# Kernel tuning notes

Hardware: AMD Instinct MI355X
Metric: run time of the kernel (lower is better)

Reference implementation:

```python
import jax, jax.numpy as jnp
import numpy as np

EMBED_DIM = 4096
NUM_Q_HEADS = 32
NUM_KV_HEADS = 8
HEAD_DIM = EMBED_DIM // NUM_Q_HEADS  # 128
GROUP = NUM_Q_HEADS // NUM_KV_HEADS  # 4
KV_SEQ_LEN = 1024
BATCH = 2
SEQ = 1024
THETA = 10000.0


def _rope(x, positions):
    # x: (B, T, H, D) with interleaved real/imag pairs along D (torch view_as_complex layout)
    half = x.shape[-1] // 2
    inv_freq = 1.0 / (THETA ** (jnp.arange(half, dtype=jnp.float32) / half))
    ang = positions[:, None].astype(jnp.float32) * inv_freq[None, :]  # (T, half)
    cos = jnp.cos(ang)[None, :, None, :].astype(x.dtype)
    sin = jnp.sin(ang)[None, :, None, :].astype(x.dtype)
    xr = x.reshape(*x.shape[:-1], half, 2)
    x0, x1 = xr[..., 0], xr[..., 1]
    o0 = x0 * cos - x1 * sin
    o1 = x0 * sin + x1 * cos
    return jnp.stack([o0, o1], axis=-1).reshape(x.shape)


def setup_inputs() -> dict:
    key = jax.random.key(0)
    ks = jax.random.split(key, 5)
    s_in = 1.0 / np.sqrt(EMBED_DIM)
    return {
        "x": jax.random.normal(ks[0], (BATCH, SEQ, EMBED_DIM), dtype=jnp.float32),
        "Wq": jax.random.normal(ks[1], (EMBED_DIM, EMBED_DIM), dtype=jnp.float32) * s_in,
        "Wk": jax.random.normal(ks[2], (NUM_KV_HEADS * HEAD_DIM, EMBED_DIM), dtype=jnp.float32) * s_in,
        "Wv": jax.random.normal(ks[3], (NUM_KV_HEADS * HEAD_DIM, EMBED_DIM), dtype=jnp.float32) * s_in,
        "Wo": jax.random.normal(ks[4], (EMBED_DIM, EMBED_DIM), dtype=jnp.float32) * s_in,
        "cache_k": jnp.zeros((BATCH, 2 * KV_SEQ_LEN, NUM_KV_HEADS, HEAD_DIM), dtype=jnp.float32),
        "cache_v": jnp.zeros((BATCH, 2 * KV_SEQ_LEN, NUM_KV_HEADS, HEAD_DIM), dtype=jnp.float32),
        "start_pos": 0,
    }


def reference(x, Wq, Wk, Wv, Wo, cache_k, cache_v, start_pos):
    B, T, C = x.shape
    end_pos = start_pos + T
    scale = 1.0 / np.sqrt(HEAD_DIM)

    q = (x @ Wq.T).reshape(B, T, NUM_Q_HEADS, HEAD_DIM)
    k = (x @ Wk.T).reshape(B, T, NUM_KV_HEADS, HEAD_DIM)
    v = (x @ Wv.T).reshape(B, T, NUM_KV_HEADS, HEAD_DIM)

    pos = start_pos + jnp.arange(T)
    q = _rope(q, pos)
    k = _rope(k, pos)

    # KV cache append (writes are detached in the original)
    cache_k = cache_k.at[:, start_pos:end_pos].set(jax.lax.stop_gradient(k))
    cache_v = cache_v.at[:, start_pos:end_pos].set(jax.lax.stop_gradient(v))
    k_full = cache_k[:, :end_pos]  # (B, S, Hkv, D)
    v_full = cache_v[:, :end_pos]

    # GQA without materializing repeated KV heads:
    # q head h attends kv head h // GROUP (matches repeat_interleave layout)
    q5 = q.transpose(0, 2, 1, 3).reshape(B, NUM_KV_HEADS, GROUP, T, HEAD_DIM)
    kh = k_full.transpose(0, 2, 1, 3)  # (B, Hkv, S, D)
    vh = v_full.transpose(0, 2, 1, 3)

    scores = jnp.einsum('bhgtd,bhsd->bhgts', q5, kh) * scale  # (B,Hkv,G,T,S)
    visible = jnp.arange(end_pos)[None, :] <= (start_pos + jnp.arange(T))[:, None]  # (T,S)
    scores = jnp.where(visible[None, None, None], scores, jnp.finfo(scores.dtype).min)
    probs = jax.nn.softmax(scores, axis=-1)
    ctx = jnp.einsum('bhgts,bhsd->bhgtd', probs, vh)

    out = ctx.reshape(B, NUM_Q_HEADS, T, HEAD_DIM).transpose(0, 2, 1, 3).reshape(B, T, C)
    return out @ Wo.T
```

## Files before the change

### kernel.cpp

```cpp
#include <hip/hip_runtime.h>
#include <stdint.h>

typedef unsigned short u16;
typedef __attribute__((ext_vector_type(8))) short short8x;
typedef __attribute__((ext_vector_type(4))) float floatx4;

#define TOKENS 2048
#define EMBED  4096
#define QKVN   6144
#define T_SEQ  1024
#define SMAX   2048
#define NQH    32
#define NKVH   8
#define HD     128

static __device__ __forceinline__ u16 f2b(float f) {
    union { float f; uint32_t u; } v; v.f = f;
    uint32_t r = v.u + 0x7fffu + ((v.u >> 16) & 1u);
    return (u16)(r >> 16);
}
static __device__ __forceinline__ float b2f(u16 h) {
    union { uint32_t u; float f; } v; v.u = ((uint32_t)h) << 16; return v.f;
}

static __device__ __forceinline__ void gload_lds16(const u16* g, u16* l) {
    __builtin_amdgcn_global_load_lds(
        (const __attribute__((address_space(1))) uint32_t*)g,
        (__attribute__((address_space(3))) uint32_t*)l, 16, 0, 0);
}

#define CSEG0 2097152
#define CSEG1 6291456
#define CSEG2 7340032
#define CSEG3 8388608
#define CSEG4 12582912
__global__ void convert_all_kernel(const float* __restrict__ x,  const float* __restrict__ Wq,
                                   const float* __restrict__ Wk, const float* __restrict__ Wv,
                                   const float* __restrict__ Wo,
                                   u16* __restrict__ xb, u16* __restrict__ wqkv,
                                   u16* __restrict__ wob) {
    int i = blockIdx.x * blockDim.x + threadIdx.x;
    if (i >= CSEG4) return;
    const float4* src; uint2* dst; int off;
    if (i < CSEG0)      { src = (const float4*)x;  dst = (uint2*)xb;   off = i; }
    else if (i < CSEG1) { src = (const float4*)Wq; dst = (uint2*)wqkv; off = i - CSEG0; }
    else if (i < CSEG2) { src = (const float4*)Wk; dst = (uint2*)wqkv + 4194304; off = i - CSEG1; }
    else if (i < CSEG3) { src = (const float4*)Wv; dst = (uint2*)wqkv + 5242880; off = i - CSEG2; }
    else                { src = (const float4*)Wo; dst = (uint2*)wob;  off = i - CSEG3; }
    float4 f = src[off];
    union { u16 h[4]; uint2 v; } o;
    o.h[0] = f2b(f.x); o.h[1] = f2b(f.y); o.h[2] = f2b(f.z); o.h[3] = f2b(f.w);
    dst[off] = o.v;
}

#define HB(BUF, MAT, H) (lds + (((BUF) * 4 + (MAT) * 2 + (H)) * 8192))
#define STAGE(BUF, MAT, H, KT) do { \
    const u16* _g0 = (MAT) ? gB[H][0] : gA[H][0]; \
    const u16* _g1 = (MAT) ? gB[H][1] : gA[H][1]; \
    gload_lds16(_g0 + (size_t)(KT) * 64, HB(BUF, MAT, H) + dOff0); \
    gload_lds16(_g1 + (size_t)(KT) * 64, HB(BUF, MAT, H) + dOff1); \
} while (0)
#define WAIT4 asm volatile("s_waitcnt vmcnt(4)" ::: "memory")
#define WAIT0 asm volatile("s_waitcnt vmcnt(0)" ::: "memory")
#define NOSTG ((void)0)
#define LDAF(CBUF, AH, KK) do { const u16* _p = HB(CBUF, 0, AH); \
    _Pragma("unroll") \
    for (int _mi = 0; _mi < 4; _mi++) \
        af[_mi] = *(const short8x*)(_p + offA[_mi][KK]); } while (0)
#define LDBF(CBUF, KK) do { \
    const u16* _p0 = HB(CBUF, 1, 0); \
    const u16* _p1 = HB(CBUF, 1, 1); \
    bf[0] = *(const short8x*)(_p0 + offB[0][KK]); \
    bf[1] = *(const short8x*)(_p0 + offB[1][KK]); \
    bf[2] = *(const short8x*)(_p1 + offB[0][KK]); \
    bf[3] = *(const short8x*)(_p1 + offB[1][KK]); } while (0)
#define NOLDB ((void)0)
#define PHASE(CBUF, AH, KK, LOADB, STAGES, ENDW) do { \
    LDAF(CBUF, AH, KK); \
    LOADB; \
    STAGES; \
    __builtin_amdgcn_s_barrier(); \
    asm volatile("s_waitcnt lgkmcnt(0)" ::: "memory"); \
    __builtin_amdgcn_sched_barrier(0); \
    __builtin_amdgcn_s_setprio(1); \
    _Pragma("unroll") \
    for (int _mi = 0; _mi < 4; _mi++) \
        _Pragma("unroll") \
        for (int _nj = 0; _nj < 4; _nj++) \
            acc[AH][_mi][_nj] = __builtin_amdgcn_mfma_f32_16x16x32_bf16( \
                af[_mi], bf[_nj], acc[AH][_mi][_nj], 0, 0, 0); \
    __builtin_amdgcn_s_setprio(0); \
    ENDW; \
    __builtin_amdgcn_s_barrier(); \
    __builtin_amdgcn_sched_barrier(0); \
} while (0)

__global__ __launch_bounds__(512, 1) void gemm256_kernel(
    const u16* __restrict__ A, const u16* __restrict__ Bw,
    u16* __restrict__ Cv, int N, int K) {
    extern __shared__ __align__(16) u16 lds[];
    const int tid = threadIdx.x;
    const int lane = tid & 63, w = tid >> 6;
    const int quad = lane >> 4, lc = lane & 15;
    const int wm = w >> 2, wn = w & 3;
    const int Mbase = blockIdx.y * 256, Nbase = blockIdx.x * 256;

    const int r8 = lane >> 3;
    const int sl = (lane & 7) ^ r8;
    const int srow = w * 8 + r8;
    const u16* gA[2][2];
    const u16* gB[2][2];
#pragma unroll
    for (int H = 0; H < 2; H++)
#pragma unroll
        for (int L = 0; L < 2; L++) {
            gA[H][L] = A  + (size_t)(Mbase + H * 128 + L * 64 + srow) * K + sl * 8;
            gB[H][L] = Bw + (size_t)(Nbase + H * 128 + L * 64 + srow) * K + sl * 8;
        }
    const int dOff0 = w * 8 * 64;
    const int dOff1 = (64 + w * 8) * 64;

    int offA[4][2], offB[2][2];
    const int xsw = lc & 7;
#pragma unroll
    for (int mi = 0; mi < 4; mi++)
#pragma unroll
        for (int kk = 0; kk < 2; kk++)
            offA[mi][kk] = (wm * 64 + mi * 16 + lc) * 64 + (((kk * 4 + quad) ^ xsw) * 8);
#pragma unroll
    for (int ni = 0; ni < 2; ni++)
#pragma unroll
        for (int kk = 0; kk < 2; kk++)
            offB[ni][kk] = (wn * 32 + ni * 16 + lc) * 64 + (((kk * 4 + quad) ^ xsw) * 8);

    floatx4 acc[2][4][4] = {};
    short8x af[4];
    short8x bf[4];

    STAGE(0, 0, 0, 0);
    STAGE(0, 1, 0, 0);
    STAGE(0, 0, 1, 0);
    STAGE(0, 1, 1, 0);
    STAGE(1, 0, 0, 1);
    STAGE(1, 1, 0, 1);
    WAIT4;
    __builtin_amdgcn_s_barrier();
    __builtin_amdgcn_sched_barrier(0);

    const int NT = K >> 6;
    for (int t = 0; t < NT - 2; t += 2) {
        PHASE(0, 0, 0, LDBF(0, 0), STAGE(1, 0, 1, t + 1); STAGE(1, 1, 1, t + 1), NOSTG);
        PHASE(0, 1, 0, NOLDB, NOSTG, NOSTG);
        PHASE(0, 0, 1, LDBF(0, 1), NOSTG, NOSTG);
        PHASE(0, 1, 1, NOLDB, STAGE(0, 0, 0, t + 2); STAGE(0, 1, 0, t + 2), WAIT4);
        PHASE(1, 0, 0, LDBF(1, 0), STAGE(0, 0, 1, t + 2); STAGE(0, 1, 1, t + 2), NOSTG);
        PHASE(1, 1, 0, NOLDB, NOSTG, NOSTG);
        PHASE(1, 0, 1, LDBF(1, 1), NOSTG, NOSTG);
        PHASE(1, 1, 1, NOLDB, STAGE(1, 0, 0, t + 3); STAGE(1, 1, 0, t + 3), WAIT4);
    }
    PHASE(0, 0, 0, LDBF(0, 0), STAGE(1, 0, 1, NT - 1); STAGE(1, 1, 1, NT - 1), NOSTG);
    PHASE(0, 1, 0, NOLDB, NOSTG, NOSTG);
    PHASE(0, 0, 1, LDBF(0, 1), NOSTG, NOSTG);
    PHASE(0, 1, 1, NOLDB, NOSTG, WAIT0);
    PHASE(1, 0, 0, LDBF(1, 0), NOSTG, NOSTG);
    PHASE(1, 1, 0, NOLDB, NOSTG, NOSTG);
    PHASE(1, 0, 1, LDBF(1, 1), NOSTG, NOSTG);
    PHASE(1, 1, 1, NOLDB, NOSTG, NOSTG);

#pragma unroll
    for (int AH = 0; AH < 2; AH++)
#pragma unroll
        for (int mi = 0; mi < 4; mi++) {
            const int row0 = Mbase + AH * 128 + wm * 64 + mi * 16 + quad * 4;
#pragma unroll
            for (int nj = 0; nj < 4; nj++) {
                const int col = Nbase + (nj >> 1) * 128 + wn * 32 + (nj & 1) * 16 + lc;
#pragma unroll
                for (int r = 0; r < 4; r++)
                    Cv[(size_t)(row0 + r) * N + col] = f2b(acc[AH][mi][nj][r]);
            }
        }
}
#undef HB
#undef STAGE
#undef LDAF
#undef LDBF
#undef NOLDB
#undef PHASE

#define HA2(BUF, H) (lds + (BUF) * 24576 + (H) * 4096)
#define HBB2(BUF)   (lds + (BUF) * 24576 + 8192)
#define STGA2(BUF, H, KT) gload_lds16(gA2[H] + (size_t)(KT) * 64, HA2(BUF, H) + dOffW)
#define STGB2(BUF, KT) do { \
    _Pragma("unroll") \
    for (int _L = 0; _L < 4; _L++) \
        gload_lds16(gB2[_L] + (size_t)(KT) * 64, HBB2(BUF) + _L * 4096 + dOffW); \
} while (0)
#define WAIT5 asm volatile("s_waitcnt vmcnt(5)" ::: "memory")
#define LDA2(CBUF, AH) do { const u16* _p = HA2(CBUF, AH); \
    _Pragma("unroll") \
    for (int _mi = 0; _mi < 2; _mi++) { \
        af2[_mi][0] = *(const short8x*)(_p + offA2[_mi][0]); \
        af2[_mi][1] = *(const short8x*)(_p + offA2[_mi][1]); } } while (0)
#define LDB2(CBUF) do { const u16* _p = HBB2(CBUF); \
    _Pragma("unroll") \
    for (int _nj = 0; _nj < 4; _nj++) { \
        bf2[_nj][0] = *(const short8x*)(_p + offB2[_nj][0]); \
        bf2[_nj][1] = *(const short8x*)(_p + offB2[_nj][1]); } } while (0)
#define PHASE2(CBUF, AH, LOADS, STAGES, ENDW) do { \
    LOADS; \
    STAGES; \
    __builtin_amdgcn_s_barrier(); \
    asm volatile("s_waitcnt lgkmcnt(0)" ::: "memory"); \
    __builtin_amdgcn_sched_barrier(0); \
    __builtin_amdgcn_s_setprio(1); \
    _Pragma("unroll") \
    for (int _kk = 0; _kk < 2; _kk++) \
        _Pragma("unroll") \
        for (int _mi = 0; _mi < 2; _mi++) \
            _Pragma("unroll") \
            for (int _nj = 0; _nj < 4; _nj++) \
                acc2[AH][_mi][_nj] = __builtin_amdgcn_mfma_f32_16x16x32_bf16( \
                    af2[_mi][_kk], bf2[_nj][_kk], acc2[AH][_mi][_nj], 0, 0, 0); \
    __builtin_amdgcn_s_setprio(0); \
    ENDW; \
    __builtin_amdgcn_s_barrier(); \
    __builtin_amdgcn_sched_barrier(0); \
} while (0)

__global__ __launch_bounds__(512, 1) void gemmko_kernel(
    const u16* __restrict__ A, const u16* __restrict__ Bw,
    float* __restrict__ C, int N, int K) {
    extern __shared__ __align__(16) u16 lds[];
    const int tid = threadIdx.x;
    const int lane = tid & 63, w = tid >> 6;
    const int quad = lane >> 4, lc = lane & 15;
    const int wm = (w >> 2) & 1, wn = w & 3;
    const int Mbase = blockIdx.y * 128, Nbase = blockIdx.x * 256;

    const int r8 = lane >> 3;
    const int sl = (lane & 7) ^ r8;
    const int srow = w * 8 + r8;
    const u16* gA2[2];
    const u16* gB2[4];
#pragma unroll
    for (int H = 0; H < 2; H++)
        gA2[H] = A + (size_t)(Mbase + H * 64 + srow) * K + sl * 8;
#pragma unroll
    for (int L = 0; L < 4; L++)
        gB2[L] = Bw + (size_t)(Nbase + L * 64 + srow) * K + sl * 8;
    const int dOffW = w * 512;

    int offA2[2][2], offB2[4][2];
    const int xsw = lc & 7;
#pragma unroll
    for (int mi = 0; mi < 2; mi++)
#pragma unroll
        for (int kk = 0; kk < 2; kk++)
            offA2[mi][kk] = (wm * 32 + mi * 16 + lc) * 64 + (((kk * 4 + quad) ^ xsw) * 8);
#pragma unroll
    for (int nj = 0; nj < 4; nj++)
#pragma unroll
        for (int kk = 0; kk < 2; kk++)
            offB2[nj][kk] = (wn * 64 + nj * 16 + lc) * 64 + (((kk * 4 + quad) ^ xsw) * 8);

    floatx4 acc2[2][2][4] = {};
    short8x af2[2][2], bf2[4][2];

    STGA2(0, 0, 0); STGA2(0, 1, 0); STGB2(0, 0);
    STGA2(1, 0, 1); STGB2(1, 1);
    WAIT5;
    __builtin_amdgcn_s_barrier();
    __builtin_amdgcn_sched_barrier(0);

    const int NT = K >> 6;
    for (int t = 0; t < NT - 2; t += 2) {
        PHASE2(0, 0, LDA2(0, 0); LDB2(0), STGA2(1, 1, t + 1), NOSTG);
        PHASE2(0, 1, LDA2(0, 1), STGA2(0, 0, t + 2); STGB2(0, t + 2), WAIT5);
        PHASE2(1, 0, LDA2(1, 0); LDB2(1), STGA2(0, 1, t + 2), NOSTG);
        PHASE2(1, 1, LDA2(1, 1), STGA2(1, 0, t + 3); STGB2(1, t + 3), WAIT5);
    }
    PHASE2(0, 0, LDA2(0, 0); LDB2(0), STGA2(1, 1, NT - 1), NOSTG);
    PHASE2(0, 1, LDA2(0, 1), NOSTG, WAIT0);
    PHASE2(1, 0, LDA2(1, 0); LDB2(1), NOSTG, NOSTG);
    PHASE2(1, 1, LDA2(1, 1), NOSTG, NOSTG);

#pragma unroll
    for (int AH = 0; AH < 2; AH++)
#pragma unroll
        for (int mi = 0; mi < 2; mi++) {
            const int row0 = Mbase + AH * 64 + wm * 32 + mi * 16 + quad * 4;
#pragma unroll
            for (int nj = 0; nj < 4; nj++) {
                const int col = Nbase + wn * 64 + nj * 16 + lc;
#pragma unroll
                for (int r = 0; r < 4; r++)
                    C[(size_t)(row0 + r) * N + col] = acc2[AH][mi][nj][r];
            }
        }
}
#undef HA2
#undef HBB2
#undef STGA2
#undef STGB2
#undef WAIT5
#undef LDA2
#undef LDB2
#undef PHASE2
#undef WAIT4
#undef WAIT0
#undef NOSTG

__global__ void cache_prefix_kernel(const float* __restrict__ ck, const float* __restrict__ cv,
                                    const int* __restrict__ sp,
                                    u16* __restrict__ kh, u16* __restrict__ vt8) {
    int spos = sp[0];
    long total = (long)2 * spos * NKVH * HD;
    for (long i = (long)blockIdx.x * blockDim.x + threadIdx.x; i < total; i += (long)gridDim.x * blockDim.x) {
        long d = i % HD, rest = i / HD;
        long g = rest % NKVH; rest /= NKVH;
        long s = rest % spos; long b = rest / spos;
        float kv = ck[((b * SMAX + s) * NKVH + g) * HD + d];
        kh[((b * NKVH + g) * SMAX + s) * HD + d] = f2b(kv);
        float vv = cv[((b * SMAX + s) * NKVH + g) * HD + d];
        vt8[(size_t)(b * NKVH + g) * SMAX * HD + (s >> 3) * 1024 + d * 8 + (s & 7)] = f2b(vv);
    }
}

__global__ void rope_qk_kernel(const u16* __restrict__ qkvb, const int* __restrict__ sp,
                               u16* __restrict__ qh, u16* __restrict__ kh) {
    int spos = sp[0];
    int idx = blockIdx.x * blockDim.x + threadIdx.x;
    int tok = idx / 2560;
    int u = idx - tok * 2560;
    int b = tok >> 10, t = tok & 1023;
    float pos = (float)(spos + t);
    const u16* src = qkvb + (size_t)tok * QKVN;
    const float kScale = 0.08838834764831845f;
    const float kLog = -0.20762050593045857f;
    if (u < 2048) {
        int h = u >> 6, i = u & 63;
        float ang = pos * exp2f((float)i * kLog);
        float cs = cosf(ang), sn = sinf(ang);
        float x0 = b2f(src[h * HD + 2 * i]), x1 = b2f(src[h * HD + 2 * i + 1]);
        size_t dst = (((size_t)(b * NQH + h) * T_SEQ) + t) * HD + 2 * i;
        qh[dst]     = f2b((x0 * cs - x1 * sn) * kScale);
        qh[dst + 1] = f2b((x0 * sn + x1 * cs) * kScale);
    } else {
        int u2 = u - 2048;
        int g = u2 >> 6, i = u2 & 63;
        float ang = pos * exp2f((float)i * kLog);
        float cs = cosf(ang), sn = sinf(ang);
        float x0 = b2f(src[EMBED + g * HD + 2 * i]), x1 = b2f(src[EMBED + g * HD + 2 * i + 1]);
        size_t dst = (((size_t)(b * NKVH + g) * SMAX) + spos + t) * HD + 2 * i;
        kh[dst]     = f2b(x0 * cs - x1 * sn);
        kh[dst + 1] = f2b(x0 * sn + x1 * cs);
    }
}

__global__ __launch_bounds__(256) void vpack_kernel(const u16* __restrict__ qkvb,
                                                    const int* __restrict__ sp,
                                                    u16* __restrict__ vt8) {
    __shared__ u16 lds[16 * 136];
    int spos = sp[0];
    int tile = blockIdx.x;
    int t16 = tile & 63;
    int g = (tile >> 6) & 7;
    int b = tile >> 9;
    int tok0 = t16 * 16;
    int tid = threadIdx.x;
    {
        int srow = tid >> 4, dc8 = (tid & 15) * 8;
        const u16* src = qkvb + (size_t)(b * T_SEQ + tok0 + srow) * QKVN + 5120 + g * HD + dc8;
        *(uint4*)(lds + srow * 136 + dc8) = *(const uint4*)src;
    }
    __syncthreads();
    int d = tid & 127, half = tid >> 7;
    u16* vpg = vt8 + (size_t)(b * NKVH + g) * SMAX * HD;
    int s0 = spos + tok0;
    u16 val[8];
#pragma unroll
    for (int k = 0; k < 8; k++) val[k] = lds[(half * 8 + k) * 136 + d];
    if ((s0 & 7) == 0) {
        union { u16 h[8]; uint4 u; } pk;
#pragma unroll
        for (int k = 0; k < 8; k++) pk.h[k] = val[k];
        *(uint4*)(vpg + (size_t)((s0 >> 3) + half) * 1024 + d * 8) = pk.u;
    } else {
#pragma unroll
        for (int k = 0; k < 8; k++) {
            int s = s0 + half * 8 + k;
            vpg[(size_t)(s >> 3) * 1024 + d * 8 + (s & 7)] = val[k];
        }
    }
}

__global__ __launch_bounds__(256, 2) void attn_kernel(
    const u16* __restrict__ qh, const u16* __restrict__ kh,
    const u16* __restrict__ vt8, const int* __restrict__ sp,
    u16* __restrict__ ctx) {
    extern __shared__ __align__(16) char smem[];
    int spos = sp[0];
    int tid = threadIdx.x, w = tid >> 6, lane = tid & 63;
    int quad = lane >> 4, lc = lane & 15;
    int tile = blockIdx.x;
    int j = 63 - (tile & 63);
    int g = (tile >> 6) & 7;
    int b = tile >> 9;
    int qbase = j * 16;

    const u16* kp = kh + (size_t)(b * NKVH + g) * SMAX * HD;
    const u16* vp = vt8 + (size_t)(b * NKVH + g) * SMAX * HD;

    short8x qf[4][4];
#pragma unroll
    for (int m = 0; m < 4; m++) {
        const u16* qp = qh + ((size_t)(b * NQH + g * 4 + m) * T_SEQ + qbase + lc) * HD + quad * 8;
#pragma unroll
        for (int dc = 0; dc < 4; dc++)
            qf[m][dc] = *(const short8x*)(qp + dc * 32);
    }
    short8x ones;
#pragma unroll
    for (int jj = 0; jj < 8; jj++) ones[jj] = (short)0x3F80;

    floatx4 o[4][8] = {};
    floatx4 lacc[4] = {};
    int rowpos = spos + qbase + quad * 4;
    int nch = (spos + qbase + 16 + 63) >> 6;
    u16* pw = (u16*)smem + w * 4608;

    for (int c = w; c < nch; c += 4) {
        int koff = c * 64;
#pragma unroll
        for (int st = 0; st < 4; st++) {
            const u16* kr = kp + (size_t)(koff + st * 16 + lc) * HD + quad * 8;
            floatx4 sc[4] = {};
#pragma unroll
            for (int dc = 0; dc < 4; dc++) {
                short8x kf = *(const short8x*)(kr + dc * 32);
#pragma unroll
                for (int m = 0; m < 4; m++)
                    sc[m] = __builtin_amdgcn_mfma_f32_16x16x32_bf16(qf[m][dc], kf, sc[m], 0, 0, 0);
            }
            int skey = koff + st * 16 + lc;
#pragma unroll
            for (int m = 0; m < 4; m++)
#pragma unroll
                for (int r = 0; r < 4; r++) {
                    float p = (skey <= rowpos + r) ? __expf(sc[m][r]) : 0.0f;
                    pw[m * 1152 + (quad * 4 + r) * 72 + st * 16 + lc] = f2b(p);
                }
        }
        asm volatile("s_waitcnt lgkmcnt(0)" ::: "memory");
#pragma unroll
        for (int hf = 0; hf < 2; hf++) {
            short8x pf[4];
#pragma unroll
            for (int m = 0; m < 4; m++)
                pf[m] = *(const short8x*)(pw + m * 1152 + lc * 72 + hf * 32 + quad * 8);
#pragma unroll
            for (int m = 0; m < 4; m++)
                lacc[m] = __builtin_amdgcn_mfma_f32_16x16x32_bf16(pf[m], ones, lacc[m], 0, 0, 0);
            const u16* vbase = vp + ((size_t)koff << 7) + (size_t)(hf * 4 + quad) * 1024 + lc * 8;
#pragma unroll
            for (int dc8 = 0; dc8 < 8; dc8++) {
                short8x vf = *(const short8x*)(vbase + dc8 * 128);
#pragma unroll
                for (int m = 0; m < 4; m++)
                    o[m][dc8] = __builtin_amdgcn_mfma_f32_16x16x32_bf16(pf[m], vf, o[m][dc8], 0, 0, 0);
            }
        }
    }

    float* obuf = (float*)smem;
    float* lbuf = (float*)(smem + 33792);
    for (int ph = 0; ph < 4; ph++) {
        __syncthreads();
        if (w == ph) {
            if (ph == 0) {
#pragma unroll
                for (int m = 0; m < 4; m++) {
#pragma unroll
                    for (int dc8 = 0; dc8 < 8; dc8++)
#pragma unroll
                        for (int r = 0; r < 4; r++)
                            obuf[(m * 16 + quad * 4 + r) * 132 + dc8 * 16 + lc] = o[m][dc8][r];
#pragma unroll
                    for (int r = 0; r < 4; r++) lbuf[m * 16 + quad * 4 + r] = lacc[m][r];
                }
            } else {
#pragma unroll
                for (int m = 0; m < 4; m++) {
#pragma unroll
                    for (int dc8 = 0; dc8 < 8; dc8++)
#pragma unroll
                        for (int r = 0; r < 4; r++)
                            obuf[(m * 16 + quad * 4 + r) * 132 + dc8 * 16 + lc] += o[m][dc8][r];
#pragma unroll
                    for (int r = 0; r < 4; r++) lbuf[m * 16 + quad * 4 + r] += lacc[m][r];
                }
            }
        }
    }
    __syncthreads();

    int row = tid >> 2;
    int m = row >> 4;
    int cb = (tid & 3) * 32;
    float inv = 1.0f / lbuf[row];
    int token = qbase + (row & 15);
    size_t base = ((size_t)(b * T_SEQ + token) * NQH + g * 4 + m) * HD + cb;
#pragma unroll
    for (int v4 = 0; v4 < 4; v4++) {
        union { u16 h[8]; uint4 u; } pk;
#pragma unroll
        for (int jj = 0; jj < 8; jj++)
            pk.h[jj] = f2b(obuf[row * 132 + cb + v4 * 8 + jj] * inv);
        *(uint4*)(ctx + base + v4 * 8) = pk.u;
    }
}

extern "C" void kernel_launch(void* const* d_in, const int* in_sizes, int n_in,
                              void* d_out, int out_size, void* d_ws, size_t ws_size,
                              hipStream_t stream) {
    const float* x  = (const float*)d_in[0];
    const float* Wq = (const float*)d_in[1];
    const float* Wk = (const float*)d_in[2];
    const float* Wv = (const float*)d_in[3];
    const float* Wo = (const float*)d_in[4];
    const float* ck = (const float*)d_in[5];
    const float* cv = (const float*)d_in[6];
    const int*   sp = (const int*)d_in[7];

    char* p = (char*)d_ws;
    u16* xb   = (u16*)p;
    u16* qh   = xb;
    p += (size_t)TOKENS * EMBED * 2;
    u16* wqkv = (u16*)p; p += (size_t)QKVN * EMBED * 2;
    u16* wob  = (u16*)p; p += (size_t)EMBED * EMBED * 2;
    u16* qkvb = (u16*)p;
    u16* ctx  = qkvb;
    p += (size_t)TOKENS * QKVN * 2;
    u16* kh   = (u16*)p; p += (size_t)2 * NKVH * SMAX * HD * 2;
    u16* vt8  = (u16*)p;

    static int gemm_attr = 0;
    if (!gemm_attr) {
        (void)hipFuncSetAttribute(reinterpret_cast<const void*>(&gemm256_kernel),
                                  hipFuncAttributeMaxDynamicSharedMemorySize, 131072);
        (void)hipFuncSetAttribute(reinterpret_cast<const void*>(&gemmko_kernel),
                                  hipFuncAttributeMaxDynamicSharedMemorySize, 98304);
        gemm_attr = 1;
    }

    convert_all_kernel<<<(CSEG4 + 255) / 256, 256, 0, stream>>>(x, Wq, Wk, Wv, Wo, xb, wqkv, wob);
    gemm256_kernel<<<dim3(QKVN / 256, TOKENS / 256), 512, 131072, stream>>>(xb, wqkv, qkvb, QKVN, EMBED);
    cache_prefix_kernel<<<256, 256, 0, stream>>>(ck, cv, sp, kh, vt8);
    rope_qk_kernel<<<TOKENS * 2560 / 256, 256, 0, stream>>>(qkvb, sp, qh, kh);
    vpack_kernel<<<1024, 256, 0, stream>>>(qkvb, sp, vt8);
    attn_kernel<<<1024, 256, 36864, stream>>>(qh, kh, vt8, sp, ctx);
    gemmko_kernel<<<dim3(EMBED / 256, TOKENS / 128), 512, 98304, stream>>>(ctx, wob, (float*)d_out, EMBED, EMBED);
}
```

Baseline: 337.2 us.

## Reshape QKV GEMM tile to 256x192 so the grid fills all CUs

Each block of the QKV projection GEMM now covers 192 output columns instead of 256. That gives a grid of 256 blocks instead of 192, so every CU on the device gets one block and the partial last wave goes away. The B-tile staging, LDS layout, fragment offsets, accumulators and epilogue are rewritten for three 64-row B slices, and the LDS allocation shrinks. Both GEMM kernels also replace the explicit lgkmcnt(0) wait and sched_barrier around barriers with compiler memory fences. That hands LDS wait placement to the compiler, trading a smaller per-block tile (less reuse) for better CU coverage.

```diff
diff --git a/kernel.cpp b/kernel.cpp
--- a/kernel.cpp
+++ b/kernel.cpp
@@ -53,46 +53,46 @@
     dst[off] = o.v;
 }
 
-#define HB(BUF, MAT, H) (lds + (((BUF) * 4 + (MAT) * 2 + (H)) * 8192))
-#define STAGE(BUF, MAT, H, KT) do { \
-    const u16* _g0 = (MAT) ? gB[H][0] : gA[H][0]; \
-    const u16* _g1 = (MAT) ? gB[H][1] : gA[H][1]; \
-    gload_lds16(_g0 + (size_t)(KT) * 64, HB(BUF, MAT, H) + dOff0); \
-    gload_lds16(_g1 + (size_t)(KT) * 64, HB(BUF, MAT, H) + dOff1); \
-} while (0)
-#define WAIT4 asm volatile("s_waitcnt vmcnt(4)" ::: "memory")
+#define FENCE asm volatile("" ::: "memory")
+#define WAIT5 asm volatile("s_waitcnt vmcnt(5)" ::: "memory")
 #define WAIT0 asm volatile("s_waitcnt vmcnt(0)" ::: "memory")
 #define NOSTG ((void)0)
-#define LDAF(CBUF, AH, KK) do { const u16* _p = HB(CBUF, 0, AH); \
+#define NOLDB ((void)0)
+
+#define HBA(BUF, H) (lds + (BUF) * 28672 + (H) * 8192)
+#define HBB(BUF)    (lds + (BUF) * 28672 + 16384)
+#define STGA(BUF, H, KT) do { \
+    gload_lds16(gA[H][0] + (size_t)(KT) * 64, HBA(BUF, H) + dOffW); \
+    gload_lds16(gA[H][1] + (size_t)(KT) * 64, HBA(BUF, H) + 4096 + dOffW); \
+} while (0)
+#define STGB(BUF, KT) do { \
+    _Pragma("unroll") \
+    for (int _L = 0; _L < 3; _L++) \
+        gload_lds16(gBv[_L] + (size_t)(KT) * 64, HBB(BUF) + _L * 4096 + dOffW); \
+} while (0)
+#define LDAF(CBUF, AH, KK) do { const u16* _p = HBA(CBUF, AH); \
     _Pragma("unroll") \
     for (int _mi = 0; _mi < 4; _mi++) \
         af[_mi] = *(const short8x*)(_p + offA[_mi][KK]); } while (0)
-#define LDBF(CBUF, KK) do { \
-    const u16* _p0 = HB(CBUF, 1, 0); \
-    const u16* _p1 = HB(CBUF, 1, 1); \
-    bf[0] = *(const short8x*)(_p0 + offB[0][KK]); \
-    bf[1] = *(const short8x*)(_p0 + offB[1][KK]); \
-    bf[2] = *(const short8x*)(_p1 + offB[0][KK]); \
-    bf[3] = *(const short8x*)(_p1 + offB[1][KK]); } while (0)
-#define NOLDB ((void)0)
+#define LDBF(CBUF, KK) do { const u16* _p = HBB(CBUF); \
+    _Pragma("unroll") \
+    for (int _nj = 0; _nj < 3; _nj++) \
+        bf[_nj] = *(const short8x*)(_p + offB[_nj][KK]); } while (0)
 #define PHASE(CBUF, AH, KK, LOADB, STAGES, ENDW) do { \
     LDAF(CBUF, AH, KK); \
     LOADB; \
     STAGES; \
-    __builtin_amdgcn_s_barrier(); \
-    asm volatile("s_waitcnt lgkmcnt(0)" ::: "memory"); \
-    __builtin_amdgcn_sched_barrier(0); \
+    FENCE; __builtin_amdgcn_s_barrier(); FENCE; \
     __builtin_amdgcn_s_setprio(1); \
     _Pragma("unroll") \
     for (int _mi = 0; _mi < 4; _mi++) \
         _Pragma("unroll") \
-        for (int _nj = 0; _nj < 4; _nj++) \
+        for (int _nj = 0; _nj < 3; _nj++) \
             acc[AH][_mi][_nj] = __builtin_amdgcn_mfma_f32_16x16x32_bf16( \
                 af[_mi], bf[_nj], acc[AH][_mi][_nj], 0, 0, 0); \
     __builtin_amdgcn_s_setprio(0); \
     ENDW; \
-    __builtin_amdgcn_s_barrier(); \
-    __builtin_amdgcn_sched_barrier(0); \
+    FENCE; __builtin_amdgcn_s_barrier(); FENCE; \
 } while (0)
 
 __global__ __launch_bounds__(512, 1) void gemm256_kernel(
@@ -103,24 +103,24 @@
     const int lane = tid & 63, w = tid >> 6;
     const int quad = lane >> 4, lc = lane & 15;
     const int wm = w >> 2, wn = w & 3;
-    const int Mbase = blockIdx.y * 256, Nbase = blockIdx.x * 256;
+    const int Mbase = blockIdx.y * 256, Nbase = blockIdx.x * 192;
 
     const int r8 = lane >> 3;
     const int sl = (lane & 7) ^ r8;
     const int srow = w * 8 + r8;
     const u16* gA[2][2];
-    const u16* gB[2][2];
+    const u16* gBv[3];
 #pragma unroll
     for (int H = 0; H < 2; H++)
 #pragma unroll
-        for (int L = 0; L < 2; L++) {
-            gA[H][L] = A  + (size_t)(Mbase + H * 128 + L * 64 + srow) * K + sl * 8;
-            gB[H][L] = Bw + (size_t)(Nbase + H * 128 + L * 64 + srow) * K + sl * 8;
-        }
-    const int dOff0 = w * 8 * 64;
-    const int dOff1 = (64 + w * 8) * 64;
-
-    int offA[4][2], offB[2][2];
+        for (int L = 0; L < 2; L++)
+            gA[H][L] = A + (size_t)(Mbase + H * 128 + L * 64 + srow) * K + sl * 8;
+#pragma unroll
+    for (int L = 0; L < 3; L++)
+        gBv[L] = Bw + (size_t)(Nbase + L * 64 + srow) * K + sl * 8;
+    const int dOffW = w * 512;
+
+    int offA[4][2], offB[3][2];
     const int xsw = lc & 7;
 #pragma unroll
     for (int mi = 0; mi < 4; mi++)
@@ -128,37 +128,32 @@
         for (int kk = 0; kk < 2; kk++)
             offA[mi][kk] = (wm * 64 + mi * 16 + lc) * 64 + (((kk * 4 + quad) ^ xsw) * 8);
 #pragma unroll
-    for (int ni = 0; ni < 2; ni++)
+    for (int nj = 0; nj < 3; nj++)
 #pragma unroll
         for (int kk = 0; kk < 2; kk++)
-            offB[ni][kk] = (wn * 32 + ni * 16 + lc) * 64 + (((kk * 4 + quad) ^ xsw) * 8);
-
-    floatx4 acc[2][4][4] = {};
+            offB[nj][kk] = (wn * 48 + nj * 16 + lc) * 64 + (((kk * 4 + quad) ^ xsw) * 8);
+
+    floatx4 acc[2][4][3] = {};
     short8x af[4];
-    short8x bf[4];
-
-    STAGE(0, 0, 0, 0);
-    STAGE(0, 1, 0, 0);
-    STAGE(0, 0, 1, 0);
-    STAGE(0, 1, 1, 0);
-    STAGE(1, 0, 0, 1);
-    STAGE(1, 1, 0, 1);
-    WAIT4;
-    __builtin_amdgcn_s_barrier();
-    __builtin_amdgcn_sched_barrier(0);
+    short8x bf[3];
+
+    STGA(0, 0, 0); STGA(0, 1, 0); STGB(0, 0);
+    STGA(1, 0, 1); STGB(1, 1);
+    WAIT5;
+    FENCE; __builtin_amdgcn_s_barrier(); FENCE;
 
     const int NT = K >> 6;
     for (int t = 0; t < NT - 2; t += 2) {
-        PHASE(0, 0, 0, LDBF(0, 0), STAGE(1, 0, 1, t + 1); STAGE(1, 1, 1, t + 1), NOSTG);
+        PHASE(0, 0, 0, LDBF(0, 0), STGA(1, 1, t + 1), NOSTG);
         PHASE(0, 1, 0, NOLDB, NOSTG, NOSTG);
         PHASE(0, 0, 1, LDBF(0, 1), NOSTG, NOSTG);
-        PHASE(0, 1, 1, NOLDB, STAGE(0, 0, 0, t + 2); STAGE(0, 1, 0, t + 2), WAIT4);
-        PHASE(1, 0, 0, LDBF(1, 0), STAGE(0, 0, 1, t + 2); STAGE(0, 1, 1, t + 2), NOSTG);
+        PHASE(0, 1, 1, NOLDB, STGA(0, 0, t + 2); STGB(0, t + 2), WAIT5);
+        PHASE(1, 0, 0, LDBF(1, 0), STGA(0, 1, t + 2), NOSTG);
         PHASE(1, 1, 0, NOLDB, NOSTG, NOSTG);
         PHASE(1, 0, 1, LDBF(1, 1), NOSTG, NOSTG);
-        PHASE(1, 1, 1, NOLDB, STAGE(1, 0, 0, t + 3); STAGE(1, 1, 0, t + 3), WAIT4);
-    }
-    PHASE(0, 0, 0, LDBF(0, 0), STAGE(1, 0, 1, NT - 1); STAGE(1, 1, 1, NT - 1), NOSTG);
+        PHASE(1, 1, 1, NOLDB, STGA(1, 0, t + 3); STGB(1, t + 3), WAIT5);
+    }
+    PHASE(0, 0, 0, LDBF(0, 0), STGA(1, 1, NT - 1), NOSTG);
     PHASE(0, 1, 0, NOLDB, NOSTG, NOSTG);
     PHASE(0, 0, 1, LDBF(0, 1), NOSTG, NOSTG);
     PHASE(0, 1, 1, NOLDB, NOSTG, WAIT0);
@@ -173,19 +168,20 @@
         for (int mi = 0; mi < 4; mi++) {
             const int row0 = Mbase + AH * 128 + wm * 64 + mi * 16 + quad * 4;
 #pragma unroll
-            for (int nj = 0; nj < 4; nj++) {
-                const int col = Nbase + (nj >> 1) * 128 + wn * 32 + (nj & 1) * 16 + lc;
+            for (int nj = 0; nj < 3; nj++) {
+                const int col = Nbase + wn * 48 + nj * 16 + lc;
 #pragma unroll
                 for (int r = 0; r < 4; r++)
                     Cv[(size_t)(row0 + r) * N + col] = f2b(acc[AH][mi][nj][r]);
             }
         }
 }
-#undef HB
-#undef STAGE
+#undef HBA
+#undef HBB
+#undef STGA
+#undef STGB
 #undef LDAF
 #undef LDBF
-#undef NOLDB
 #undef PHASE
 
 #define HA2(BUF, H) (lds + (BUF) * 24576 + (H) * 4096)
@@ -196,7 +192,7 @@
     for (int _L = 0; _L < 4; _L++) \
         gload_lds16(gB2[_L] + (size_t)(KT) * 64, HBB2(BUF) + _L * 4096 + dOffW); \
 } while (0)
-#define WAIT5 asm volatile("s_waitcnt vmcnt(5)" ::: "memory")
+#define WAIT5K asm volatile("s_waitcnt vmcnt(5)" ::: "memory")
 #define LDA2(CBUF, AH) do { const u16* _p = HA2(CBUF, AH); \
     _Pragma("unroll") \
     for (int _mi = 0; _mi < 2; _mi++) { \
@@ -210,9 +206,7 @@
 #define PHASE2(CBUF, AH, LOADS, STAGES, ENDW) do { \
     LOADS; \
     STAGES; \
-    __builtin_amdgcn_s_barrier(); \
-    asm volatile("s_waitcnt lgkmcnt(0)" ::: "memory"); \
-    __builtin_amdgcn_sched_barrier(0); \
+    FENCE; __builtin_amdgcn_s_barrier(); FENCE; \
     __builtin_amdgcn_s_setprio(1); \
     _Pragma("unroll") \
     for (int _kk = 0; _kk < 2; _kk++) \
@@ -224,8 +218,7 @@
                     af2[_mi][_kk], bf2[_nj][_kk], acc2[AH][_mi][_nj], 0, 0, 0); \
     __builtin_amdgcn_s_setprio(0); \
     ENDW; \
-    __builtin_amdgcn_s_barrier(); \
-    __builtin_amdgcn_sched_barrier(0); \
+    FENCE; __builtin_amdgcn_s_barrier(); FENCE; \
 } while (0)
 
 __global__ __launch_bounds__(512, 1) void gemmko_kernel(
@@ -269,16 +262,15 @@
 
     STGA2(0, 0, 0); STGA2(0, 1, 0); STGB2(0, 0);
     STGA2(1, 0, 1); STGB2(1, 1);
-    WAIT5;
-    __builtin_amdgcn_s_barrier();
-    __builtin_amdgcn_sched_barrier(0);
+    WAIT5K;
+    FENCE; __builtin_amdgcn_s_barrier(); FENCE;
 
     const int NT = K >> 6;
     for (int t = 0; t < NT - 2; t += 2) {
         PHASE2(0, 0, LDA2(0, 0); LDB2(0), STGA2(1, 1, t + 1), NOSTG);
-        PHASE2(0, 1, LDA2(0, 1), STGA2(0, 0, t + 2); STGB2(0, t + 2), WAIT5);
+        PHASE2(0, 1, LDA2(0, 1), STGA2(0, 0, t + 2); STGB2(0, t + 2), WAIT5K);
         PHASE2(1, 0, LDA2(1, 0); LDB2(1), STGA2(0, 1, t + 2), NOSTG);
-        PHASE2(1, 1, LDA2(1, 1), STGA2(1, 0, t + 3); STGB2(1, t + 3), WAIT5);
+        PHASE2(1, 1, LDA2(1, 1), STGA2(1, 0, t + 3); STGB2(1, t + 3), WAIT5K);
     }
     PHASE2(0, 0, LDA2(0, 0); LDB2(0), STGA2(1, 1, NT - 1), NOSTG);
     PHASE2(0, 1, LDA2(0, 1), NOSTG, WAIT0);
@@ -303,13 +295,15 @@
 #undef HBB2
 #undef STGA2
 #undef STGB2
-#undef WAIT5
+#undef WAIT5K
 #undef LDA2
 #undef LDB2
 #undef PHASE2
-#undef WAIT4
+#undef WAIT5
 #undef WAIT0
 #undef NOSTG
+#undef NOLDB
+#undef FENCE
 
 __global__ void cache_prefix_kernel(const float* __restrict__ ck, const float* __restrict__ cv,
                                     const int* __restrict__ sp,
@@ -548,14 +542,14 @@
     static int gemm_attr = 0;
     if (!gemm_attr) {
         (void)hipFuncSetAttribute(reinterpret_cast<const void*>(&gemm256_kernel),
-                                  hipFuncAttributeMaxDynamicSharedMemorySize, 131072);
+                                  hipFuncAttributeMaxDynamicSharedMemorySize, 114688);
         (void)hipFuncSetAttribute(reinterpret_cast<const void*>(&gemmko_kernel),
                                   hipFuncAttributeMaxDynamicSharedMemorySize, 98304);
         gemm_attr = 1;
     }
 
     convert_all_kernel<<<(CSEG4 + 255) / 256, 256, 0, stream>>>(x, Wq, Wk, Wv, Wo, xb, wqkv, wob);
-    gemm256_kernel<<<dim3(QKVN / 256, TOKENS / 256), 512, 131072, stream>>>(xb, wqkv, qkvb, QKVN, EMBED);
+    gemm256_kernel<<<dim3(QKVN / 192, TOKENS / 256), 512, 114688, stream>>>(xb, wqkv, qkvb, QKVN, EMBED);
     cache_prefix_kernel<<<256, 256, 0, stream>>>(ck, cv, sp, kh, vt8);
     rope_qk_kernel<<<TOKENS * 2560 / 256, 256, 0, stream>>>(qkvb, sp, qh, kh);
     vpack_kernel<<<1024, 256, 0, stream>>>(qkvb, sp, vt8);
```

Result: faster. 322.4 us (-4.4%).
